# Kernel optimization log

Measured on AMD Instinct MI355X. Metric: run time of the kernel, lower is better.

## Reference

```python
import jax, jax.numpy as jnp
import numpy as np

EPS = 1e-5

def _conv1x1(x, w, b):
    # x: [B,C,H,W], w: [O,C], b: [O] -> [B,O,H,W]
    return jnp.einsum('bchw,oc->bohw', x, w) + b[None, :, None, None]

def setup_inputs() -> dict:
    key = jax.random.key(0)
    ks = jax.random.split(key, 13)
    B, C, H, W = 16, 256, 64, 64
    Ci = C // 2
    s = 0.05
    return {
        'x': jax.random.normal(ks[0], (B, C, H, W), jnp.float32),
        'g_w': jax.random.normal(ks[1], (Ci, C), jnp.float32) * s,
        'g_b': jax.random.normal(ks[2], (Ci,), jnp.float32) * s,
        'theta_w': jax.random.normal(ks[3], (Ci, C), jnp.float32) * s,
        'theta_b': jax.random.normal(ks[4], (Ci,), jnp.float32) * s,
        'phi_w': jax.random.normal(ks[5], (Ci, C), jnp.float32) * s,
        'phi_b': jax.random.normal(ks[6], (Ci,), jnp.float32) * s,
        'w_w': jax.random.normal(ks[7], (C, Ci), jnp.float32) * s,
        'w_b': jax.random.normal(ks[8], (C,), jnp.float32) * s,
        'bn_gamma': jax.random.normal(ks[9], (C,), jnp.float32),
        'bn_beta': jax.random.normal(ks[10], (C,), jnp.float32),
        'bn_mean': jax.random.normal(ks[11], (C,), jnp.float32),
        'bn_var': jax.random.uniform(ks[12], (C,), jnp.float32, 0.5, 1.5),
    }

def reference(x, g_w, g_b, theta_w, theta_b, phi_w, phi_b,
              w_w, w_b, bn_gamma, bn_beta, bn_mean, bn_var):
    B, C, H, W = x.shape
    N = H * W
    Ci = g_w.shape[0]
    # 1x1 conv projections, flatten spatial to N
    g_x = _conv1x1(x, g_w, g_b).reshape(B, Ci, N).transpose(0, 2, 1)        # [B,N,Ci]
    theta_x = _conv1x1(x, theta_w, theta_b).reshape(B, Ci, N).transpose(0, 2, 1)  # [B,N,Ci]
    phi_x = _conv1x1(x, phi_w, phi_b).reshape(B, Ci, N)                     # [B,Ci,N]
    # affinity f = theta @ phi, normalized by N (softmax-free linear attention)
    f_div_C = jnp.einsum('bnc,bcm->bnm', theta_x, phi_x) / N                # [B,N,N]
    y = jnp.einsum('bnm,bmc->bnc', f_div_C, g_x)                            # [B,N,Ci]
    y = y.transpose(0, 2, 1).reshape(B, Ci, H, W)
    # W: 1x1 conv + BatchNorm (eval mode, running stats)
    w_y = _conv1x1(y, w_w, w_b)
    inv = bn_gamma * jax.lax.rsqrt(bn_var + EPS)
    w_y = w_y * inv[None, :, None, None] + (bn_beta - bn_mean * inv)[None, :, None, None]
    return w_y + x
```

## Files before the change

### kernel.cpp

```cpp
#include <hip/hip_runtime.h>
#include <stdint.h>

#define BATCH 16
#define CH    256
#define CI    128
#define NSP   4096
#define KC    8
#define EPSV  1e-5f

typedef unsigned short u16;
typedef __attribute__((ext_vector_type(4))) float f32x4;
typedef __attribute__((ext_vector_type(8))) short bf16x8;

__device__ __forceinline__ u16 f2b(float f) {
  uint32_t u = __float_as_uint(f);
  uint32_t r = u + 0x7FFFu + ((u >> 16) & 1u);
  return (u16)(r >> 16);
}

__device__ __forceinline__ void async16(void* lds, const void* g) {
  __builtin_amdgcn_global_load_lds(
      (const __attribute__((address_space(1))) unsigned int*)g,
      (__attribute__((address_space(3))) unsigned int*)lds, 16, 0, 0);
}

__global__ __launch_bounds__(256) void k_const(const float* __restrict__ w_w,
    const float* __restrict__ g_w, const float* __restrict__ g_b,
    const float* __restrict__ theta_w, const float* __restrict__ theta_b,
    const float* __restrict__ phi_w, const float* __restrict__ phi_b,
    const float* __restrict__ w_b, const float* __restrict__ bn_g,
    const float* __restrict__ bn_b, const float* __restrict__ bn_m,
    const float* __restrict__ bn_v,
    float* __restrict__ E, float* __restrict__ KT, float* __restrict__ wg,
    float* __restrict__ tphi, float* __restrict__ q, float* __restrict__ inv,
    float* __restrict__ dconst, float* __restrict__ tb) {
  __shared__ float lbuf[1024];
  const int blk = blockIdx.x, t = threadIdx.x;
  if (blk < 32) {
    const int o0 = blk*8;
    #pragma unroll
    for (int k = 0; k < 4; ++k) { int idx = k*256 + t;
      lbuf[idx] = w_w[(size_t)(o0 + (idx & 7))*CI + (idx >> 3)]; }
    __syncthreads();
    float acc[8] = {0.f};
    for (int j = 0; j < CI; ++j) {
      float gv = g_w[(size_t)j*CH + t];
      #pragma unroll
      for (int r = 0; r < 8; ++r) acc[r] += lbuf[j*8 + r] * gv;
    }
    #pragma unroll
    for (int r = 0; r < 8; ++r) E[(size_t)(o0 + r)*CH + t] = acc[r];
  } else if (blk < 64) {
    const int a0 = (blk - 32)*8;
    #pragma unroll
    for (int k = 0; k < 4; ++k) { int idx = k*256 + t;
      lbuf[idx] = phi_w[(size_t)(idx >> 3)*CH + a0 + (idx & 7)]; }
    __syncthreads();
    float acc[8] = {0.f};
    for (int i = 0; i < CI; ++i) {
      float tv = theta_w[(size_t)i*CH + t];
      #pragma unroll
      for (int u = 0; u < 8; ++u) acc[u] += lbuf[i*8 + u] * tv;
    }
    #pragma unroll
    for (int u = 0; u < 8; ++u) KT[(size_t)(a0 + u)*CH + t] = acc[u];
  } else {
    float iv = bn_g[t] * rsqrtf(bn_v[t] + EPSV);
    inv[t] = iv;
    dconst[t] = iv*w_b[t] + bn_b[t] - bn_m[t]*iv;
    float a = 0.f;
    for (int j = 0; j < CI; ++j) a += w_w[(size_t)t*CI + j] * g_b[j];
    wg[t] = a;
    float tp = 0.f, qq = 0.f;
    for (int i = 0; i < CI; ++i) {
      tp += theta_w[(size_t)i*CH + t] * phi_b[i];
      qq += phi_w[(size_t)i*CH + t] * theta_b[i];
    }
    tphi[t] = tp; q[t] = qq;
    lbuf[t] = (t < CI) ? theta_b[t]*phi_b[t] : 0.f;
    __syncthreads();
    for (int s2 = 128; s2 > 0; s2 >>= 1) { if (t < s2) lbuf[t] += lbuf[t + s2]; __syncthreads(); }
    if (t == 0) tb[0] = lbuf[0];
  }
}

__global__ __launch_bounds__(256) void k_prep(const float* __restrict__ x,
    u16* __restrict__ xb, u16* __restrict__ xt, float* __restrict__ psum) {
  __shared__ float tile[64*64];
  const int b = blockIdx.z, c0 = blockIdx.y*64, n0 = blockIdx.x*64;
  const int t = threadIdx.x;
  const int lane16 = t & 15;
  const int grp = t >> 4;
  const float* xp = x + ((size_t)b*CH + c0)*NSP + n0;
  u16* xbp = xb + ((size_t)b*CH + c0)*NSP + n0;
  #pragma unroll
  for (int p = 0; p < 4; ++p) {
    int cl = grp + p*16;
    int nl = lane16*4;
    float4 v = *(const float4*)(xp + (size_t)cl*NSP + nl);
    float ps = v.x + v.y + v.z + v.w;
    #pragma unroll
    for (int o = 1; o < 16; o <<= 1) ps += __shfl_xor(ps, o, 64);
    if (lane16 == 0) psum[((size_t)b*64 + blockIdx.x)*CH + c0 + cl] = ps;
    ushort4 bv; bv.x=f2b(v.x); bv.y=f2b(v.y); bv.z=f2b(v.z); bv.w=f2b(v.w);
    *(ushort4*)(xbp + (size_t)cl*NSP + nl) = bv;
    float vv[4] = {v.x, v.y, v.z, v.w};
    #pragma unroll
    for (int j = 0; j < 4; ++j) {
      int n = nl + j;
      tile[n*64 + (cl ^ (((n>>2)&7)<<2))] = vv[j];
    }
  }
  __syncthreads();
  u16* xtp = xt + ((size_t)b*NSP + n0)*CH + c0;
  #pragma unroll
  for (int q2 = 0; q2 < 4; ++q2) {
    int nl = grp + q2*16;
    int c4 = lane16*4;
    float4 v = *(const float4*)&tile[nl*64 + (c4 ^ (((nl>>2)&7)<<2))];
    ushort4 bv; bv.x=f2b(v.x); bv.y=f2b(v.y); bv.z=f2b(v.z); bv.w=f2b(v.w);
    *(ushort4*)(xtp + (size_t)nl*CH + c4) = bv;
  }
}

__global__ __launch_bounds__(256) void k_gram(const u16* __restrict__ xb, float* __restrict__ Sp) {
  __shared__ u16 As[128*64];
  __shared__ u16 Bs[128*64];
  const int L = blockIdx.x;
  const int wk = (L & 7) * 48 + (L >> 3);
  const int b = wk / 24;
  const int rem = wk % 24;
  const int kc = rem / 3;
  const int q = rem % 3;
  const int m_base = (q == 2) ? 128 : 0;
  const int n_base = (q == 0) ? 0 : 128;
  const int t = threadIdx.x, wv = t >> 6, l = t & 63;
  const int wr = wv >> 1, wc = wv & 1;
  const int lr = l & 15, lkb = l >> 4;
  const int sr = l >> 3, ss = l & 7;
  const u16* xa = xb + (size_t)b*CH*NSP;
  const int kbeg = kc * (NSP/KC);
  f32x4 acc[4][4];
  #pragma unroll
  for (int i = 0; i < 4; ++i)
    #pragma unroll
    for (int j = 0; j < 4; ++j) acc[i][j] = (f32x4){0.f,0.f,0.f,0.f};

  for (int kk = 0; kk < 8; ++kk) {
    const int kpos = kbeg + kk*64;
    #pragma unroll
    for (int j4 = 0; j4 < 4; ++j4) {
      const int j = wv*4 + j4;
      const int r = j*8 + sr;
      async16(&As[j*512], xa + (size_t)(m_base + r)*NSP + kpos + ((ss ^ (r & 7)) * 8));
    }
    if (q == 1) {
      #pragma unroll
      for (int j4 = 0; j4 < 4; ++j4) {
        const int j = wv*4 + j4;
        const int r = j*8 + sr;
        async16(&Bs[j*512], xa + (size_t)(n_base + r)*NSP + kpos + ((ss ^ (r & 7)) * 8));
      }
    }
    __syncthreads();
    const u16* bsrc = (q == 1) ? Bs : As;
    #pragma unroll
    for (int ks = 0; ks < 2; ++ks) {
      bf16x8 A[4], Bf[4];
      #pragma unroll
      for (int mt = 0; mt < 4; ++mt) {
        const int ra = wr*64 + mt*16 + lr;
        A[mt] = *(const bf16x8*)(As + ra*64 + (((ks*4 + lkb) ^ (ra & 7)) * 8));
      }
      #pragma unroll
      for (int nt = 0; nt < 4; ++nt) {
        const int rb = wc*64 + nt*16 + lr;
        Bf[nt] = *(const bf16x8*)(bsrc + rb*64 + (((ks*4 + lkb) ^ (rb & 7)) * 8));
      }
      #pragma unroll
      for (int mt = 0; mt < 4; ++mt)
        #pragma unroll
        for (int nt = 0; nt < 4; ++nt)
          acc[mt][nt] = __builtin_amdgcn_mfma_f32_16x16x32_bf16(A[mt], Bf[nt], acc[mt][nt], 0, 0, 0);
    }
    __syncthreads();
  }
  float* Sb = Sp + (size_t)(b*KC + kc)*CH*CH;
  const int r0 = (l >> 4) * 4;
  #pragma unroll
  for (int mt = 0; mt < 4; ++mt)
    #pragma unroll
    for (int nt = 0; nt < 4; ++nt)
      #pragma unroll
      for (int rr = 0; rr < 4; ++rr)
        Sb[(size_t)(m_base + wr*64 + mt*16 + r0 + rr)*CH + n_base + wc*64 + nt*16 + lr]
          = acc[mt][nt][rr];
}

__global__ __launch_bounds__(256) void k_red(const float* __restrict__ Sp, float* __restrict__ S) {
  __shared__ float tl[64*65];
  const int b = blockIdx.y, tt = blockIdx.x, t = threadIdx.x;
  const int qq = tt >> 2, sub = tt & 3;
  const int qi = (qq == 2) ? 1 : 0, qj = (qq == 0) ? 0 : 1;
  const int row0 = qi*128 + (sub >> 1)*64, col0 = qj*128 + (sub & 1)*64;
  const float* p = Sp + (size_t)b*KC*CH*CH;
  float* Sb = S + (size_t)b*CH*CH;
  float4 sum[4];
  #pragma unroll
  for (int k = 0; k < 4; ++k) {
    const int slot = t + k*256;
    const int r = slot >> 4, c4 = (slot & 15) * 4;
    float4 s = {0.f,0.f,0.f,0.f};
    #pragma unroll
    for (int kc = 0; kc < KC; ++kc) {
      float4 v = *(const float4*)(p + (size_t)kc*CH*CH + (size_t)(row0 + r)*CH + col0 + c4);
      s.x += v.x; s.y += v.y; s.z += v.z; s.w += v.w;
    }
    sum[k] = s;
    *(float4*)(Sb + (size_t)(row0 + r)*CH + col0 + c4) = s;
  }
  if (qq == 1) {
    #pragma unroll
    for (int k = 0; k < 4; ++k) {
      const int slot = t + k*256;
      const int r = slot >> 4, c4 = (slot & 15) * 4;
      tl[r*65 + c4+0] = sum[k].x; tl[r*65 + c4+1] = sum[k].y;
      tl[r*65 + c4+2] = sum[k].z; tl[r*65 + c4+3] = sum[k].w;
    }
    __syncthreads();
    #pragma unroll
    for (int k = 0; k < 4; ++k) {
      const int slot = t + k*256;
      const int r = slot >> 4, c4 = (slot & 15) * 4;
      float4 v = { tl[(c4+0)*65 + r], tl[(c4+1)*65 + r], tl[(c4+2)*65 + r], tl[(c4+3)*65 + r] };
      *(float4*)(Sb + (size_t)(col0 + r)*CH + row0 + c4) = v;
    }
  }
}

__global__ __launch_bounds__(256) void k_vec2(const float* __restrict__ psum,
    const float* __restrict__ E, const float* __restrict__ KT,
    const float* __restrict__ q, float* __restrict__ KS, float* __restrict__ Es,
    float* __restrict__ qs) {
  __shared__ float ls[CH];
  __shared__ float rbuf[4];
  const int b = blockIdx.x, t = threadIdx.x;
  float s = 0.f;
  for (int xb = 0; xb < 64; ++xb) s += psum[((size_t)b*64 + xb)*CH + t];
  ls[t] = s;
  __syncthreads();
  float ks = 0.f;
  for (int a = 0; a < CH; ++a) ks += KT[(size_t)a*CH + t] * ls[a];
  KS[(size_t)b*CH + t] = ks;
  float es = 0.f;
  for (int c = 0; c < CH; ++c) es += E[(size_t)t*CH + c] * ls[c];
  Es[(size_t)b*CH + t] = es;
  float p = q[t] * ls[t];
  #pragma unroll
  for (int o = 1; o < 64; o <<= 1) p += __shfl_xor(p, o, 64);
  if ((t & 63) == 0) rbuf[t >> 6] = p;
  __syncthreads();
  if (t == 0) qs[b] = rbuf[0] + rbuf[1] + rbuf[2] + rbuf[3];
}

__global__ __launch_bounds__(256) void k_R(const float* __restrict__ S,
    const float* __restrict__ E, const float* __restrict__ q,
    float* __restrict__ R, float* __restrict__ Rq) {
  __shared__ float lEt[2048];
  __shared__ float red[32];
  const int b = blockIdx.y, o0 = blockIdx.x*8, t = threadIdx.x;
  #pragma unroll
  for (int k = 0; k < 8; ++k) { int idx = k*256 + t;
    lEt[idx] = E[(size_t)(o0 + (idx & 7))*CH + (idx >> 3)]; }
  __syncthreads();
  const float* Sb = S + (size_t)b*CH*CH;
  float acc[8] = {0.f};
  for (int c = 0; c < CH; ++c) {
    float sv = Sb[(size_t)c*CH + t];
    #pragma unroll
    for (int r = 0; r < 8; ++r) acc[r] += lEt[c*8 + r] * sv;
  }
  float* Rb = R + (size_t)b*CH*CH;
  #pragma unroll
  for (int r = 0; r < 8; ++r) Rb[(size_t)(o0 + r)*CH + t] = acc[r];
  const float qt = q[t];
  #pragma unroll
  for (int r = 0; r < 8; ++r) {
    float p = acc[r] * qt;
    #pragma unroll
    for (int o = 1; o < 64; o <<= 1) p += __shfl_xor(p, o, 64);
    if ((t & 63) == 0) red[r*4 + (t >> 6)] = p;
  }
  __syncthreads();
  if (t < 8) {
    float sum = red[t*4] + red[t*4+1] + red[t*4+2] + red[t*4+3];
    Rq[(size_t)b*CH + o0 + t] = sum;
  }
}

__global__ __launch_bounds__(256) void k_P(const float* __restrict__ R,
    const float* __restrict__ KT, const float* __restrict__ Rq,
    const float* __restrict__ KS, const float* __restrict__ Es,
    const float* __restrict__ qs, const float* __restrict__ wg,
    const float* __restrict__ tphi, const float* __restrict__ inv,
    const float* __restrict__ dconst, const float* __restrict__ tb,
    u16* __restrict__ Pb, float* __restrict__ dv) {
  __shared__ float lRt[2048];
  const int b = blockIdx.y, o0 = blockIdx.x*8, t = threadIdx.x;
  const float* Rb = R + (size_t)b*CH*CH;
  #pragma unroll
  for (int k = 0; k < 8; ++k) { int idx = k*256 + t;
    lRt[idx] = Rb[(size_t)(o0 + (idx & 7))*CH + (idx >> 3)]; }
  __syncthreads();
  float acc[8] = {0.f};
  for (int a = 0; a < CH; ++a) {
    float kv = KT[(size_t)a*CH + t];
    #pragma unroll
    for (int r = 0; r < 8; ++r) acc[r] += lRt[a*8 + r] * kv;
  }
  const float ksv = KS[(size_t)b*CH + t], tpv = tphi[t];
  u16* Pbb = Pb + (size_t)b*CH*CH;
  #pragma unroll
  for (int r = 0; r < 8; ++r) {
    int o = o0 + r;
    float val = (acc[r] + wg[o]*ksv + (Es[(size_t)b*CH + o] + (float)NSP*wg[o])*tpv)
                * inv[o] * (1.f/(float)NSP);
    Pbb[(size_t)o*CH + t] = f2b(val);
  }
  if (t < 8) {
    int o = o0 + t;
    float iv = inv[o], wgo = wg[o], tb0 = tb[0];
    float t2 = Rq[(size_t)b*CH + o] + wgo*qs[b] + Es[(size_t)b*CH + o]*tb0;
    dv[(size_t)b*CH + o] = iv*(t2*(1.f/(float)NSP) + wgo*tb0) + dconst[o];
  }
}

__global__ __launch_bounds__(512, 4) void k_apply(const u16* __restrict__ Pb,
    const u16* __restrict__ xt, const float* __restrict__ x,
    const float* __restrict__ dv, float* __restrict__ out) {
  __shared__ u16 xs[64*256];
  const int b = blockIdx.y, n0 = blockIdx.x*64;
  const int t = threadIdx.x, w = t >> 6, l = t & 63;
  {
    const u16* src = xt + ((size_t)b*NSP + n0)*CH;
    const int r = t >> 3, sbase = t & 7;
    #pragma unroll
    for (int it = 0; it < 4; ++it) {
      int slot = sbase + it*8;
      bf16x8 v = *(const bf16x8*)(src + (size_t)r*CH + slot*8);
      *(bf16x8*)(xs + r*256 + ((slot ^ (r & 7)) * 8)) = v;
    }
  }
  __syncthreads();
  const int m0 = w*32;
  const int lr = l & 15, lkb = l >> 4;
  const int sw = lr & 7;
  const u16* Pp = Pb + (size_t)b*CH*CH;
  f32x4 acc[2][4];
  #pragma unroll
  for (int i = 0; i < 2; ++i)
    #pragma unroll
    for (int j = 0; j < 4; ++j) acc[i][j] = (f32x4){0.f,0.f,0.f,0.f};
  #pragma unroll
  for (int kk = 0; kk < 8; ++kk) {
    bf16x8 A[2], Bf[4];
    #pragma unroll
    for (int mt = 0; mt < 2; ++mt)
      A[mt] = *(const bf16x8*)(Pp + (size_t)(m0 + mt*16 + lr)*CH + kk*32 + lkb*8);
    #pragma unroll
    for (int nt = 0; nt < 4; ++nt) {
      int slot = kk*4 + lkb;
      Bf[nt] = *(const bf16x8*)(xs + (nt*16 + lr)*256 + ((slot ^ sw) * 8));
    }
    #pragma unroll
    for (int mt = 0; mt < 2; ++mt)
      #pragma unroll
      for (int nt = 0; nt < 4; ++nt)
        acc[mt][nt] = __builtin_amdgcn_mfma_f32_16x16x32_bf16(A[mt], Bf[nt], acc[mt][nt], 0, 0, 0);
  }
  const float* xpb = x + (size_t)b*CH*NSP;
  float* ob = out + (size_t)b*CH*NSP;
  const int r0 = (l >> 4) * 4;
  #pragma unroll
  for (int mt = 0; mt < 2; ++mt)
    #pragma unroll
    for (int rr = 0; rr < 4; ++rr) {
      int row = m0 + mt*16 + r0 + rr;
      float dval = dv[(size_t)b*CH + row];
      #pragma unroll
      for (int nt = 0; nt < 4; ++nt) {
        int col = n0 + nt*16 + lr;
        ob[(size_t)row*NSP + col] = acc[mt][nt][rr] + xpb[(size_t)row*NSP + col] + dval;
      }
    }
}

static constexpr size_t XT_OFF = 0;
static constexpr size_t S_OFF  = 33554432;
static constexpr size_t PB_OFF = 37748736;
static constexpr size_t PS_OFF = 39845888;
static constexpr size_t E_OFF  = 40894464;
static constexpr size_t KT_OFF = 41156608;
static constexpr size_t WG_OFF = 41418752;
static constexpr size_t TP_OFF = 41419776;
static constexpr size_t QV_OFF = 41420800;
static constexpr size_t IV_OFF = 41421824;
static constexpr size_t DC_OFF = 41422848;
static constexpr size_t TB_OFF = 41423872;
static constexpr size_t KS_OFF = 41424896;
static constexpr size_t ES_OFF = 41441280;
static constexpr size_t RQ_OFF = 41457664;
static constexpr size_t QS_OFF = 41474048;
static constexpr size_t DV_OFF = 41475072;

extern "C" void kernel_launch(void* const* d_in, const int* in_sizes, int n_in,
                              void* d_out, int out_size, void* d_ws, size_t ws_size,
                              hipStream_t stream) {
  const float* x       = (const float*)d_in[0];
  const float* g_w     = (const float*)d_in[1];
  const float* g_b     = (const float*)d_in[2];
  const float* theta_w = (const float*)d_in[3];
  const float* theta_b = (const float*)d_in[4];
  const float* phi_w   = (const float*)d_in[5];
  const float* phi_b   = (const float*)d_in[6];
  const float* w_w     = (const float*)d_in[7];
  const float* w_b     = (const float*)d_in[8];
  const float* bn_g    = (const float*)d_in[9];
  const float* bn_b    = (const float*)d_in[10];
  const float* bn_m    = (const float*)d_in[11];
  const float* bn_v    = (const float*)d_in[12];
  float* out = (float*)d_out;
  char* ws = (char*)d_ws;
  u16*   XT = (u16*)(ws + XT_OFF);
  float* S  = (float*)(ws + S_OFF);
  u16*   Pb = (u16*)(ws + PB_OFF);
  float* PS = (float*)(ws + PS_OFF);
  float* E  = (float*)(ws + E_OFF);
  float* KT = (float*)(ws + KT_OFF);
  float* WG = (float*)(ws + WG_OFF);
  float* TP = (float*)(ws + TP_OFF);
  float* QV = (float*)(ws + QV_OFF);
  float* IV = (float*)(ws + IV_OFF);
  float* DC = (float*)(ws + DC_OFF);
  float* TB = (float*)(ws + TB_OFF);
  float* KS = (float*)(ws + KS_OFF);
  float* ES = (float*)(ws + ES_OFF);
  float* RQ = (float*)(ws + RQ_OFF);
  float* QS = (float*)(ws + QS_OFF);
  float* DV = (float*)(ws + DV_OFF);
  u16*   Xb = (u16*)d_out;
  float* Sp = (float*)((char*)d_out + 33554432);
  float* R  = (float*)((char*)d_out + 33554432);

  k_const<<<dim3(65),                    256, 0, stream>>>(w_w, g_w, g_b, theta_w, theta_b,
                                                           phi_w, phi_b, w_b, bn_g, bn_b, bn_m, bn_v,
                                                           E, KT, WG, TP, QV, IV, DC, TB);
  k_prep <<<dim3(NSP/64, CH/64, BATCH),  256, 0, stream>>>(x, Xb, XT, PS);
  k_gram <<<dim3(384),                   256, 0, stream>>>(Xb, Sp);
  k_red  <<<dim3(12, BATCH),             256, 0, stream>>>(Sp, S);
  k_vec2 <<<dim3(BATCH),                 256, 0, stream>>>(PS, E, KT, QV, KS, ES, QS);
  k_R    <<<dim3(32, BATCH),             256, 0, stream>>>(S, E, QV, R, RQ);
  k_P    <<<dim3(32, BATCH),             256, 0, stream>>>(R, KT, RQ, KS, ES, QS, WG, TP, IV, DC, TB, Pb, DV);
  k_apply<<<dim3(NSP/64, BATCH),         512, 0, stream>>>(Pb, XT, x, DV, out);
}
```

Baseline: 142.6 us.

## Fold residual into projection matrix as identity and fuse R/P kernels

Adds 1 to the diagonal of the per-batch projection matrix P so the residual x is produced by the MFMA GEMM over the bf16 transposed input. This removes the fp32 re-read of x in the apply kernel. The two small R and P kernels are merged into one: R stays in LDS instead of going through global memory, and the Rq reduction is consumed in place, which saves a launch and a round trip. The apply kernel's launch bounds are raised to allow more resident blocks per CU. The trade-off is accuracy: the residual now passes through bf16, and small P entries lose precision next to the unit diagonal.

New measurement: 136.4 us. 1.05x faster.

```diff
diff --git a/kernel.cpp b/kernel.cpp
--- a/kernel.cpp
+++ b/kernel.cpp
@@ -263,10 +263,15 @@
   if (t == 0) qs[b] = rbuf[0] + rbuf[1] + rbuf[2] + rbuf[3];
 }
 
-__global__ __launch_bounds__(256) void k_R(const float* __restrict__ S,
-    const float* __restrict__ E, const float* __restrict__ q,
-    float* __restrict__ R, float* __restrict__ Rq) {
+__global__ __launch_bounds__(256) void k_RP(const float* __restrict__ S,
+    const float* __restrict__ E, const float* __restrict__ KT,
+    const float* __restrict__ q, const float* __restrict__ KS,
+    const float* __restrict__ Es, const float* __restrict__ qs,
+    const float* __restrict__ wg, const float* __restrict__ tphi,
+    const float* __restrict__ inv, const float* __restrict__ dconst,
+    const float* __restrict__ tb, u16* __restrict__ Pb, float* __restrict__ dv) {
   __shared__ float lEt[2048];
+  __shared__ float lRt[2048];
   __shared__ float red[32];
   const int b = blockIdx.y, o0 = blockIdx.x*8, t = threadIdx.x;
   #pragma unroll
@@ -280,9 +285,8 @@
     #pragma unroll
     for (int r = 0; r < 8; ++r) acc[r] += lEt[c*8 + r] * sv;
   }
-  float* Rb = R + (size_t)b*CH*CH;
-  #pragma unroll
-  for (int r = 0; r < 8; ++r) Rb[(size_t)(o0 + r)*CH + t] = acc[r];
+  #pragma unroll
+  for (int r = 0; r < 8; ++r) lRt[t*8 + r] = acc[r];
   const float qt = q[t];
   #pragma unroll
   for (int r = 0; r < 8; ++r) {
@@ -292,52 +296,34 @@
     if ((t & 63) == 0) red[r*4 + (t >> 6)] = p;
   }
   __syncthreads();
-  if (t < 8) {
-    float sum = red[t*4] + red[t*4+1] + red[t*4+2] + red[t*4+3];
-    Rq[(size_t)b*CH + o0 + t] = sum;
-  }
-}
-
-__global__ __launch_bounds__(256) void k_P(const float* __restrict__ R,
-    const float* __restrict__ KT, const float* __restrict__ Rq,
-    const float* __restrict__ KS, const float* __restrict__ Es,
-    const float* __restrict__ qs, const float* __restrict__ wg,
-    const float* __restrict__ tphi, const float* __restrict__ inv,
-    const float* __restrict__ dconst, const float* __restrict__ tb,
-    u16* __restrict__ Pb, float* __restrict__ dv) {
-  __shared__ float lRt[2048];
-  const int b = blockIdx.y, o0 = blockIdx.x*8, t = threadIdx.x;
-  const float* Rb = R + (size_t)b*CH*CH;
-  #pragma unroll
-  for (int k = 0; k < 8; ++k) { int idx = k*256 + t;
-    lRt[idx] = Rb[(size_t)(o0 + (idx & 7))*CH + (idx >> 3)]; }
-  __syncthreads();
-  float acc[8] = {0.f};
+  float acc2[8] = {0.f};
   for (int a = 0; a < CH; ++a) {
     float kv = KT[(size_t)a*CH + t];
     #pragma unroll
-    for (int r = 0; r < 8; ++r) acc[r] += lRt[a*8 + r] * kv;
+    for (int r = 0; r < 8; ++r) acc2[r] += lRt[a*8 + r] * kv;
   }
   const float ksv = KS[(size_t)b*CH + t], tpv = tphi[t];
   u16* Pbb = Pb + (size_t)b*CH*CH;
   #pragma unroll
   for (int r = 0; r < 8; ++r) {
     int o = o0 + r;
-    float val = (acc[r] + wg[o]*ksv + (Es[(size_t)b*CH + o] + (float)NSP*wg[o])*tpv)
+    float val = (acc2[r] + wg[o]*ksv + (Es[(size_t)b*CH + o] + (float)NSP*wg[o])*tpv)
                 * inv[o] * (1.f/(float)NSP);
+    if (o == t) val += 1.f;
     Pbb[(size_t)o*CH + t] = f2b(val);
   }
   if (t < 8) {
     int o = o0 + t;
     float iv = inv[o], wgo = wg[o], tb0 = tb[0];
-    float t2 = Rq[(size_t)b*CH + o] + wgo*qs[b] + Es[(size_t)b*CH + o]*tb0;
+    float rq = red[t*4] + red[t*4+1] + red[t*4+2] + red[t*4+3];
+    float t2 = rq + wgo*qs[b] + Es[(size_t)b*CH + o]*tb0;
     dv[(size_t)b*CH + o] = iv*(t2*(1.f/(float)NSP) + wgo*tb0) + dconst[o];
   }
 }
 
-__global__ __launch_bounds__(512, 4) void k_apply(const u16* __restrict__ Pb,
-    const u16* __restrict__ xt, const float* __restrict__ x,
-    const float* __restrict__ dv, float* __restrict__ out) {
+__global__ __launch_bounds__(512, 8) void k_apply(const u16* __restrict__ Pb,
+    const u16* __restrict__ xt, const float* __restrict__ dv,
+    float* __restrict__ out) {
   __shared__ u16 xs[64*256];
   const int b = blockIdx.y, n0 = blockIdx.x*64;
   const int t = threadIdx.x, w = t >> 6, l = t & 63;
@@ -378,7 +364,6 @@
       for (int nt = 0; nt < 4; ++nt)
         acc[mt][nt] = __builtin_amdgcn_mfma_f32_16x16x32_bf16(A[mt], Bf[nt], acc[mt][nt], 0, 0, 0);
   }
-  const float* xpb = x + (size_t)b*CH*NSP;
   float* ob = out + (size_t)b*CH*NSP;
   const int r0 = (l >> 4) * 4;
   #pragma unroll
@@ -390,7 +375,7 @@
       #pragma unroll
       for (int nt = 0; nt < 4; ++nt) {
         int col = n0 + nt*16 + lr;
-        ob[(size_t)row*NSP + col] = acc[mt][nt][rr] + xpb[(size_t)row*NSP + col] + dval;
+        ob[(size_t)row*NSP + col] = acc[mt][nt][rr] + dval;
       }
     }
 }
@@ -409,9 +394,8 @@
 static constexpr size_t TB_OFF = 41423872;
 static constexpr size_t KS_OFF = 41424896;
 static constexpr size_t ES_OFF = 41441280;
-static constexpr size_t RQ_OFF = 41457664;
-static constexpr size_t QS_OFF = 41474048;
-static constexpr size_t DV_OFF = 41475072;
+static constexpr size_t QS_OFF = 41457664;
+static constexpr size_t DV_OFF = 41458688;
 
 extern "C" void kernel_launch(void* const* d_in, const int* in_sizes, int n_in,
                               void* d_out, int out_size, void* d_ws, size_t ws_size,
@@ -445,12 +429,10 @@
   float* TB = (float*)(ws + TB_OFF);
   float* KS = (float*)(ws + KS_OFF);
   float* ES = (float*)(ws + ES_OFF);
-  float* RQ = (float*)(ws + RQ_OFF);
   float* QS = (float*)(ws + QS_OFF);
   float* DV = (float*)(ws + DV_OFF);
   u16*   Xb = (u16*)d_out;
   float* Sp = (float*)((char*)d_out + 33554432);
-  float* R  = (float*)((char*)d_out + 33554432);
 
   k_const<<<dim3(65),                    256, 0, stream>>>(w_w, g_w, g_b, theta_w, theta_b,
                                                            phi_w, phi_b, w_b, bn_g, bn_b, bn_m, bn_v,
@@ -459,7 +441,6 @@
   k_gram <<<dim3(384),                   256, 0, stream>>>(Xb, Sp);
   k_red  <<<dim3(12, BATCH),             256, 0, stream>>>(Sp, S);
   k_vec2 <<<dim3(BATCH),                 256, 0, stream>>>(PS, E, KT, QV, KS, ES, QS);
-  k_R    <<<dim3(32, BATCH),             256, 0, stream>>>(S, E, QV, R, RQ);
-  k_P    <<<dim3(32, BATCH),             256, 0, stream>>>(R, KT, RQ, KS, ES, QS, WG, TP, IV, DC, TB, Pb, DV);
-  k_apply<<<dim3(NSP/64, BATCH),         512, 0, stream>>>(Pb, XT, x, DV, out);
-}
+  k_RP   <<<dim3(32, BATCH),             256, 0, stream>>>(S, E, KT, QV, KS, ES, QS, WG, TP, IV, DC, TB, Pb, DV);
+  k_apply<<<dim3(NSP/64, BATCH),         512, 0, stream>>>(Pb, XT, DV, out);
+}
```
